# Kernel tuning notes

Hardware: AMD Instinct MI355X
Metric: run time of the kernel (lower is better)

## Reference

```python
import jax, jax.numpy as jnp
import numpy as np
import math

S, B, D_MODEL = 1024, 2, 1024
N_HEADS = 16
D_HEAD = D_MODEL // N_HEADS
C = 32  # compressed_len


def _xavier(key, shape):
    fan_in, fan_out = shape[-1], shape[-2] if len(shape) > 1 else shape[-1]
    limit = math.sqrt(6.0 / (fan_in + fan_out))
    return jax.random.uniform(key, shape, jnp.float32, -limit, limit)


def setup_inputs() -> dict:
    key = jax.random.key(0)
    ks = jax.random.split(key, 10)
    return {
        "x": jax.random.normal(ks[0], (S, B, D_MODEL), jnp.float32),
        "q_down": _xavier(ks[1], (C, D_MODEL)),
        "Wq": _xavier(ks[2], (D_MODEL, D_MODEL)),
        "bq": jnp.zeros((D_MODEL,), jnp.float32),
        "Wk": _xavier(ks[3], (D_MODEL, D_MODEL)),
        "bk": jnp.zeros((D_MODEL,), jnp.float32),
        "Wv": _xavier(ks[4], (D_MODEL, D_MODEL)),
        "bv": jnp.zeros((D_MODEL,), jnp.float32),
        "Wo": _xavier(ks[5], (D_MODEL, D_MODEL)),
        "bo": jnp.zeros((D_MODEL,), jnp.float32),
    }


def reference(x, q_down, Wq, bq, Wk, bk, Wv, bv, Wo, bo):
    # x: (s, b, d_model); causal=True, rope=None, dropout inactive (eval)
    s, b, d_model = x.shape
    h, dh = N_HEADS, D_HEAD
    scale = 1.0 / math.sqrt(dh)

    q_u = x @ Wq.T + bq                       # (s,b,dm)
    k_d = x @ Wk.T + bk
    v_d = x @ Wv.T + bv
    v_d_k = v_d @ Wk.T + bk
    v_d_v = v_d @ Wv.T + bv

    def heads(t):  # (s,b,dm) -> (b,h,s,dh)
        return t.reshape(s, b, h, dh).transpose(1, 2, 0, 3)

    q_u = heads(q_u) * scale
    k_d = heads(k_d)
    v_d_kv = jnp.concatenate([heads(v_d_k), heads(v_d_v)], axis=-1)  # (b,h,s,2dh)

    q_d = q_down.reshape(C, h, dh).transpose(1, 0, 2) * scale        # (h,c,dh)

    down = jnp.einsum('hcd,bhsd->bhcs', q_d, k_d)                    # (b,h,c,s)
    w = jnp.exp(down - jnp.max(down, axis=-1, keepdims=True))
    norm = jnp.cumsum(w, axis=-1)

    # (b,h,c,s,2dh): running compressed KV state
    kv_u = jnp.cumsum(w[..., None] * v_d_kv[:, :, None, :, :], axis=3) / norm[..., None]
    k_u, v_u = jnp.split(kv_u, 2, axis=-1)                           # each (b,h,c,s,dh)

    up = jnp.einsum('bhsd,bhcsd->bhsc', q_u, k_u)
    up = jax.nn.softmax(up, axis=-1)
    out = jnp.einsum('bhsc,bhcsd->bhsd', up, v_u)                    # (b,h,s,dh)

    out = out.transpose(2, 0, 1, 3).reshape(s, b, d_model)
    return out @ Wo.T + bo
```

## Files before the change

kernel.cpp:

```cpp
#include <hip/hip_runtime.h>
#include <cstdint>
#include <cstddef>

#define S_LEN 1024
#define BATCH 2
#define DM    1024
#define NH    16
#define DH    64
#define CC    32
#define SB    2048
#define TSD   128
#define NCHD  8

using short8 = __attribute__((ext_vector_type(8))) short;
using f32x4  = __attribute__((ext_vector_type(4))) float;

__device__ __forceinline__ float b2f(unsigned short u) {
    union { unsigned int i; float f; } v; v.i = ((unsigned int)u) << 16; return v.f;
}
__device__ __forceinline__ unsigned short f2b(float f) {
    union { float f; unsigned int i; } v; v.f = f;
    unsigned int x = v.i;
    unsigned int r = x + 0x7FFFu + ((x >> 16) & 1u);
    return (unsigned short)(r >> 16);
}
// ... 199 lines not shown
        __syncthreads();
    }

    const int f32o = (ga.mode == 0) ? 1 : (ga.mode == 1) ? 0 : (!isbf);
    const float sc = ga.scale;
#pragma unroll
    for (int j = 0; j < 2; ++j) {
        int col = n0 + wx * 32 + j * 16 + ln;
        float bv = ga.bias[col];
#pragma unroll
        for (int i = 0; i < 4; ++i) {
            int row0 = m0 + wy * 64 + i * 16 + lq * 4;
#pragma unroll
            for (int r = 0; r < 4; ++r) {
                float v = (acc[i][j][r] + bv) * sc;
                size_t idx = (size_t)(row0 + r) * N + col;
                if (f32o) ((float*)ga.out)[idx] = v;
                else      ((unsigned short*)ga.out)[idx] = f2b(v);
            }
        }
    }
}

__global__ __launch_bounds__(256) void k_down(const unsigned short* __restrict__ kd,
                                              const unsigned short* __restrict__ qd0,
                                              const unsigned short* __restrict__ qd1,
                                              const int* __restrict__ flag,
                                              float* __restrict__ wbuf,
                                              float* __restrict__ cmax,
                                              float* __restrict__ csum)
{
    const unsigned short* qdw = (*flag) ? qd1 : qd0;
    const int bh = blockIdx.x;
    const int b = bh >> 4, h = bh & 15;
    const int chunk = blockIdx.y;
    const int s0 = chunk * TSD;
    const int t = threadIdx.x;
    const int w = t >> 6, l = t & 63;
    const int ln = l & 15, lq = l >> 4;

    __shared__ __align__(16) unsigned short QD[32 * 72];
    __shared__ __align__(16) unsigned short KT[128 * 72];
    __shared__ float SS[32 * 132];
    __shared__ float pm[256];
    __shared__ float cmf[CC];

    {
        int r = t >> 3, cb = (t & 7) * 8;
        *(short8*)&QD[r * 72 + cb] = *(const short8*)&qdw[(size_t)r * DM + h * DH + cb];
    }
    for (int u = t; u < 128 * 8; u += 256) {
        int r = u >> 3, cb = (u & 7) * 8;
        *(short8*)&KT[r * 72 + cb] =
            *(const short8*)&kd[(size_t)((s0 + r) * BATCH + b) * DM + h * DH + cb];
    }
    __syncthreads();

    f32x4 accG[2][2] = {};
#pragma unroll
    for (int ks = 0; ks < 2; ++ks) {
        short8 a8[2], b8[2];
#pragma unroll
        for (int i = 0; i < 2; ++i)
            a8[i] = *(const short8*)&QD[(i * 16 + ln) * 72 + ks * 32 + lq * 8];
#pragma unroll
        for (int j = 0; j < 2; ++j)
            b8[j] = *(const short8*)&KT[(w * 32 + j * 16 + ln) * 72 + ks * 32 + lq * 8];
#pragma unroll
        for (int i = 0; i < 2; ++i)
#pragma unroll
            for (int j = 0; j < 2; ++j)
                accG[i][j] = __builtin_amdgcn_mfma_f32_16x16x32_bf16(a8[i], b8[j], accG[i][j], 0, 0, 0);
    }
#pragma unroll
    for (int i = 0; i < 2; ++i) {
#pragma unroll
        for (int j = 0; j < 2; ++j) {
            int sl = w * 32 + j * 16 + ln;
#pragma unroll
            for (int r = 0; r < 4; ++r) {
                int c = i * 16 + lq * 4 + r;
                float v = accG[i][j][r] * 0.125f;
                SS[c * 132 + sl] = v;
                wbuf[((size_t)bh * CC + c) * S_LEN + s0 + sl] = v;
            }
        }
    }
    __syncthreads();

    const int c = t >> 3, sub = t & 7;
    float lmax = -3.4e38f;
#pragma unroll
    for (int k = 0; k < 16; ++k) lmax = fmaxf(lmax, SS[c * 132 + sub * 16 + k]);
    lmax = fmaxf(lmax, __shfl_xor(lmax, 1));
    lmax = fmaxf(lmax, __shfl_xor(lmax, 2));
    lmax = fmaxf(lmax, __shfl_xor(lmax, 4));
    if (sub == 0) {
        cmf[c] = lmax;
        cmax[((size_t)bh * CC + c) * NCHD + chunk] = lmax;
    }
    __syncthreads();
    const float cm = cmf[c];
    float es = 0.f;
#pragma unroll
    for (int k = 0; k < 16; ++k) es += __expf(SS[c * 132 + sub * 16 + k] - cm);
    es += __shfl_xor(es, 1);
    es += __shfl_xor(es, 2);
    es += __shfl_xor(es, 4);
    if (sub == 0) csum[((size_t)bh * CC + c) * NCHD + chunk] = es;
}

__global__ __launch_bounds__(256) void k_wapply(const float* __restrict__ wbuf,
                                                const float* __restrict__ cmax,
                                                const float* __restrict__ csum,
                                                unsigned short* __restrict__ wb,
                                                unsigned short* __restrict__ wT,
                                                float* __restrict__ invn)
{
    const int bh = blockIdx.x, seg = blockIdx.y;
    const int t = threadIdx.x;
    __shared__ float gm[CC];
    __shared__ float basep[CC];
    __shared__ float psum[CC][9];
    __shared__ unsigned short wTt[128 * 40];
    __shared__ float invt[128 * 36];

    if (t < CC) {
        const size_t cb = (size_t)(bh * CC + t) * NCHD;
        float m = cmax[cb];
#pragma unroll
        for (int g = 1; g < NCHD; ++g) m = fmaxf(m, cmax[cb + g]);
        gm[t] = m;
        float bsum = 0.f;
        for (int k = 0; k < seg; ++k)
            bsum += csum[cb + k] * __expf(cmax[cb + k] - m);
        basep[t] = bsum;
    }
    __syncthreads();

    const int c = t >> 3, sub = t & 7;
    const float gmc = gm[c];
    const size_t rbase = (size_t)bh * 32768 + c * 1024 + seg * 128 + sub * 16;
    float w16[16];
    float s = 0.f;
#pragma unroll
    for (int i = 0; i < 16; ++i) {
        float v = __expf(wbuf[rbase + i] - gmc);
        w16[i] = v; s += v;
    }
    psum[c][sub] = s;
    short8 o0, o1;
#pragma unroll
    for (int i = 0; i < 8; ++i) { o0[i] = f2b(w16[i]); o1[i] = f2b(w16[8 + i]); }
    *(short8*)&wb[rbase] = o0;
    *(short8*)&wb[rbase + 8] = o1;
#pragma unroll
    for (int i = 0; i < 16; ++i) wTt[(sub * 16 + i) * 40 + c] = f2b(w16[i]);
    __syncthreads();

    float run = basep[c];
    for (int k = 0; k < sub; ++k) run += psum[c][k];
#pragma unroll
    for (int i = 0; i < 16; ++i) {
        run += w16[i];
        invt[(sub * 16 + i) * 36 + c] = 1.0f / fmaxf(run, 1e-30f);
    }
    __syncthreads();

    for (int u = t; u < 128 * 4; u += 256) {
        int r = u >> 2, cb = (u & 3) * 8;
        *(short8*)&wT[(size_t)bh * 32768 + (seg * 128 + r) * 32 + cb] =
            *(const short8*)&wTt[r * 40 + cb];
    }
    for (int u = t; u < 128 * 8; u += 256) {
        int r = u >> 3, cb = (u & 7) * 4;
        *(float4*)&invn[(size_t)bh * 32768 + (seg * 128 + r) * 32 + cb] =
            *(const float4*)&invt[r * 36 + cb];
    }
}

__global__ __launch_bounds__(256) void k_state(const unsigned short* __restrict__ wb,
                                               const unsigned short* __restrict__ vdk,
                                               const unsigned short* __restrict__ vdv,
                                               float* __restrict__ Mst,
                                               float* __restrict__ NTst)
{
    const int bh = blockIdx.x, ch = blockIdx.y;
    const int b = bh >> 4, h = bh & 15;
    const int s0 = ch * 64;
    const int t = threadIdx.x;
    const int w = t >> 6, l = t & 63;
    const int ln = l & 15, lq = l >> 4;
    __shared__ __align__(16) unsigned short Ws[32 * 72];
    __shared__ __align__(16) unsigned short T1[64 * 72];
    __shared__ __align__(16) unsigned short T2[64 * 72];
    __shared__ __align__(16) unsigned short KT[64 * 72];
    __shared__ __align__(16) unsigned short VT[64 * 72];

    for (int u = t; u < 32 * 8; u += 256) {
        int r = u >> 3, cb = (u & 7) * 8;
        *(short8*)&Ws[r * 72 + cb] = *(const short8*)&wb[(size_t)bh * 32768 + r * 1024 + s0 + cb];
    }
    for (int u = t; u < 64 * 8; u += 256) {
        int r = u >> 3, cb = (u & 7) * 8;
        *(short8*)&T1[r * 72 + cb] =
            *(const short8*)&vdk[(size_t)((s0 + r) * BATCH + b) * DM + h * DH + cb];
        *(short8*)&T2[r * 72 + cb] =
            *(const short8*)&vdv[(size_t)((s0 + r) * BATCH + b) * DM + h * DH + cb];
    }
    __syncthreads();
    for (int u = t; u < 64 * 8; u += 256) {
        int d = u >> 3, s8 = (u & 7) * 8;
        short8 o1, o2;
#pragma unroll
        for (int k = 0; k < 8; ++k) {
            o1[k] = T1[(s8 + k) * 72 + d];
            o2[k] = T2[(s8 + k) * 72 + d];
        }
        *(short8*)&KT[d * 72 + s8] = o1;
        *(short8*)&VT[d * 72 + s8] = o2;
    }
    __syncthreads();

    f32x4 accM[2] = {};
#pragma unroll
    for (int ks = 0; ks < 2; ++ks) {
        short8 b8 = *(const short8*)&KT[(w * 16 + ln) * 72 + ks * 32 + lq * 8];
#pragma unroll
        for (int i = 0; i < 2; ++i) {
            short8 a8 = *(const short8*)&Ws[(i * 16 + ln) * 72 + ks * 32 + lq * 8];
            accM[i] = __builtin_amdgcn_mfma_f32_16x16x32_bf16(a8, b8, accM[i], 0, 0, 0);
        }
    }
#pragma unroll
    for (int i = 0; i < 2; ++i)
#pragma unroll
        for (int r = 0; r < 4; ++r)
            Mst[((size_t)(bh * 16 + ch) * 32 + i * 16 + lq * 4 + r) * 64 + w * 16 + ln] = accM[i][r];

    f32x4 accN[2] = {};
#pragma unroll
    for (int ks = 0; ks < 2; ++ks) {
        short8 a8 = *(const short8*)&VT[(w * 16 + ln) * 72 + ks * 32 + lq * 8];
#pragma unroll
        for (int j = 0; j < 2; ++j) {
            short8 b8 = *(const short8*)&Ws[(j * 16 + ln) * 72 + ks * 32 + lq * 8];
            accN[j] = __builtin_amdgcn_mfma_f32_16x16x32_bf16(a8, b8, accN[j], 0, 0, 0);
        }
    }
#pragma unroll
    for (int j = 0; j < 2; ++j)
#pragma unroll
        for (int r = 0; r < 4; ++r)
            NTst[((size_t)(bh * 16 + ch) * 64 + w * 16 + lq * 4 + r) * 32 + j * 16 + ln] = accN[j][r];
}

__global__ __launch_bounds__(256) void k_prefix(const float* __restrict__ Mst,
                                                const float* __restrict__ NTst,
                                                unsigned short* __restrict__ Mcum,
                                                unsigned short* __restrict__ NTcum)
{
    const int bh = blockIdx.x;
    const float* src = blockIdx.y ? NTst : Mst;
    unsigned short* dst = blockIdx.y ? NTcum : Mcum;
    const int e0 = blockIdx.z * 512 + threadIdx.x * 2;
    float r0 = 0.f, r1 = 0.f;
#pragma unroll
    for (int ch = 0; ch < 16; ++ch) {
        size_t off = (size_t)(bh * 16 + ch) * 2048 + e0;
        ushort2 ob; ob.x = f2b(r0); ob.y = f2b(r1);
        *(ushort2*)&dst[off] = ob;
        float2 v = *(const float2*)&src[off];
        r0 += v.x; r1 += v.y;
    }
}

__global__ __launch_bounds__(256) void k_att(
    const unsigned short* __restrict__ qu,
    const unsigned short* __restrict__ vdk,
    const unsigned short* __restrict__ wb,
    const float* __restrict__ invn,
    const unsigned short* __restrict__ wT,
    const unsigned short* __restrict__ vdv,
    const unsigned short* __restrict__ Mcum,
    const unsigned short* __restrict__ NTcum,
    unsigned short* __restrict__ attout)
{
    const int bh = blockIdx.x, b = bh >> 4, h = bh & 15;
    const int qi = blockIdx.y;
    const int s0 = qi * 64;
    const int t = threadIdx.x;
    const int w = t >> 6, l = t & 63;
    const int wy = w >> 1, wx = w & 1;
    const int ln = l & 15, lq = l >> 4;

    __shared__ __align__(16) unsigned short Qs[64 * 72];
    __shared__ __align__(16) unsigned short Gs[64 * 72];
    __shared__ __align__(16) unsigned short Kd[64 * 72];
    __shared__ __align__(16) unsigned short Wd[32 * 72];
    __shared__ __align__(16) unsigned short WTd[64 * 40];
    __shared__ __align__(16) unsigned short VTd[64 * 72];
    __shared__ __align__(16) unsigned short Mc[32 * 72];
    __shared__ __align__(16) unsigned short Nc[64 * 40];

    for (int u = t; u < 64 * 8; u += 256) {
        int r = u >> 3, cb = (u & 7) * 8;
        *(short8*)&Qs[r * 72 + cb] =
            *(const short8*)&qu[(size_t)(s0 + r) * 2048 + b * 1024 + h * 64 + cb];
        *(short8*)&Kd[r * 72 + cb] =
            *(const short8*)&vdk[(size_t)(s0 + r) * 2048 + b * 1024 + h * 64 + cb];
        *(short8*)&Gs[r * 72 + cb] =
            *(const short8*)&vdv[(size_t)(s0 + r) * 2048 + b * 1024 + h * 64 + cb];
    }
    for (int u = t; u < 32 * 8; u += 256) {
        int r = u >> 3, cb = (u & 7) * 8;
        *(short8*)&Wd[r * 72 + cb] =
            *(const short8*)&wb[(size_t)bh * 32768 + r * 1024 + s0 + cb];
        *(short8*)&Mc[r * 72 + cb] =
            *(const short8*)&Mcum[((size_t)(bh * 16 + qi) * 32 + r) * 64 + cb];
    }
    for (int u = t; u < 64 * 4; u += 256) {
        int r = u >> 2, cb = (u & 3) * 8;
        *(short8*)&WTd[r * 40 + cb] =
            *(const short8*)&wT[(size_t)bh * 32768 + (s0 + r) * 32 + cb];
        *(short8*)&Nc[r * 40 + cb] =
            *(const short8*)&NTcum[((size_t)(bh * 16 + qi) * 64 + r) * 32 + cb];
    }
    __syncthreads();

    for (int u = t; u < 64 * 8; u += 256) {
        int d = u >> 3, s8 = (u & 7) * 8;
        short8 o;
#pragma unroll
        for (int k = 0; k < 8; ++k) o[k] = Gs[(s8 + k) * 72 + d];
        *(short8*)&VTd[d * 72 + s8] = o;
    }
    __syncthreads();

    {
        f32x4 accG[2][2] = {};
#pragma unroll
        for (int ks = 0; ks < 2; ++ks) {
            short8 a8[2], b8[2];
#pragma unroll
            for (int i = 0; i < 2; ++i)
                a8[i] = *(const short8*)&Qs[(wy * 32 + i * 16 + ln) * 72 + ks * 32 + lq * 8];
#pragma unroll
            for (int j = 0; j < 2; ++j)
                b8[j] = *(const short8*)&Kd[(wx * 32 + j * 16 + ln) * 72 + ks * 32 + lq * 8];
#pragma unroll
            for (int i = 0; i < 2; ++i)
#pragma unroll
                for (int j = 0; j < 2; ++j)
                    accG[i][j] = __builtin_amdgcn_mfma_f32_16x16x32_bf16(a8[i], b8[j], accG[i][j], 0, 0, 0);
        }
        __syncthreads();
#pragma unroll
        for (int i = 0; i < 2; ++i) {
            int row = wy * 32 + i * 16 + lq * 4;
#pragma unroll
            for (int j = 0; j < 2; ++j) {
                int col = wx * 32 + j * 16 + ln;
#pragma unroll
                for (int r = 0; r < 4; ++r) {
                    float v = accG[i][j][r];
                    if (col > row + r) v = 0.f;
                    Gs[(row + r) * 72 + col] = f2b(v);
                }
            }
        }
    }
    __syncthreads();

    f32x4 accU[2] = {};
#pragma unroll
    for (int ks = 0; ks < 2; ++ks) {
        short8 ga = *(const short8*)&Gs[(w * 16 + ln) * 72 + ks * 32 + lq * 8];
        short8 qa = *(const short8*)&Qs[(w * 16 + ln) * 72 + ks * 32 + lq * 8];
#pragma unroll
        for (int j = 0; j < 2; ++j) {
            short8 wf = *(const short8*)&Wd[(j * 16 + ln) * 72 + ks * 32 + lq * 8];
            short8 mf = *(const short8*)&Mc[(j * 16 + ln) * 72 + ks * 32 + lq * 8];
            accU[j] = __builtin_amdgcn_mfma_f32_16x16x32_bf16(ga, wf, accU[j], 0, 0, 0);
            accU[j] = __builtin_amdgcn_mfma_f32_16x16x32_bf16(qa, mf, accU[j], 0, 0, 0);
        }
    }
    __syncthreads();

    {
        int rowl = w * 16 + lq * 4;
#pragma unroll
        for (int r = 0; r < 4; ++r) {
            int srow = s0 + rowl + r;
            float inv0 = invn[(size_t)bh * 32768 + srow * 32 + ln];
            float inv1 = invn[(size_t)bh * 32768 + srow * 32 + 16 + ln];
            float l0 = accU[0][r] * inv0;
            float l1 = accU[1][r] * inv1;
            float m = fmaxf(l0, l1);
#pragma unroll
            for (int msk = 1; msk < 16; msk <<= 1) m = fmaxf(m, __shfl_xor(m, msk));
            float e0 = __expf(l0 - m), e1 = __expf(l1 - m);
            float Z = e0 + e1;
#pragma unroll
            for (int msk = 1; msk < 16; msk <<= 1) Z += __shfl_xor(Z, msk);
            float iz = 1.0f / Z;
            Qs[(rowl + r) * 40 + ln]      = f2b(e0 * iz * inv0);
            Qs[(rowl + r) * 40 + 16 + ln] = f2b(e1 * iz * inv1);
        }
    }
    __syncthreads();

    short8 pa[2];
#pragma unroll
    for (int i = 0; i < 2; ++i)
        pa[i] = *(const short8*)&Qs[(wy * 32 + i * 16 + ln) * 40 + lq * 8];
    {
        f32x4 accS[2][2] = {};
        short8 b8[2];
#pragma unroll
        for (int j = 0; j < 2; ++j)
            b8[j] = *(const short8*)&WTd[(wx * 32 + j * 16 + ln) * 40 + lq * 8];
#pragma unroll
        for (int i = 0; i < 2; ++i)
#pragma unroll
            for (int j = 0; j < 2; ++j)
                accS[i][j] = __builtin_amdgcn_mfma_f32_16x16x32_bf16(pa[i], b8[j], accS[i][j], 0, 0, 0);
#pragma unroll
        for (int i = 0; i < 2; ++i) {
            int row = wy * 32 + i * 16 + lq * 4;
#pragma unroll
            for (int j = 0; j < 2; ++j) {
                int col = wx * 32 + j * 16 + ln;
#pragma unroll
                for (int r = 0; r < 4; ++r) {
                    float v = accS[i][j][r];
                    if (col > row + r) v = 0.f;
                    Gs[(row + r) * 72 + col] = f2b(v);
                }
            }
        }
    }
    __syncthreads();

    {
        f32x4 accO[2][2] = {};
        short8 n8[2];
#pragma unroll
        for (int j = 0; j < 2; ++j)
            n8[j] = *(const short8*)&Nc[(wx * 32 + j * 16 + ln) * 40 + lq * 8];
#pragma unroll
        for (int i = 0; i < 2; ++i)
#pragma unroll
            for (int j = 0; j < 2; ++j)
                accO[i][j] = __builtin_amdgcn_mfma_f32_16x16x32_bf16(pa[i], n8[j], accO[i][j], 0, 0, 0);
#pragma unroll
        for (int ks = 0; ks < 2; ++ks) {
            short8 a8[2], b8[2];
#pragma unroll
            for (int i = 0; i < 2; ++i)
                a8[i] = *(const short8*)&Gs[(wy * 32 + i * 16 + ln) * 72 + ks * 32 + lq * 8];
#pragma unroll
            for (int j = 0; j < 2; ++j)
                b8[j] = *(const short8*)&VTd[(wx * 32 + j * 16 + ln) * 72 + ks * 32 + lq * 8];
#pragma unroll
            for (int i = 0; i < 2; ++i)
#pragma unroll
                for (int j = 0; j < 2; ++j)
                    accO[i][j] = __builtin_amdgcn_mfma_f32_16x16x32_bf16(a8[i], b8[j], accO[i][j], 0, 0, 0);
        }
#pragma unroll
        for (int i = 0; i < 2; ++i) {
            int rowb = s0 + wy * 32 + i * 16 + lq * 4;
#pragma unroll
            for (int j = 0; j < 2; ++j) {
                int d = wx * 32 + j * 16 + ln;
#pragma unroll
                for (int r = 0; r < 4; ++r)
                    attout[(size_t)(rowb + r) * 2048 + b * 1024 + h * 64 + d] = f2b(accO[i][j][r]);
            }
        }
    }
}

extern "C" void kernel_launch(void* const* d_in, const int* in_sizes, int n_in,
                              void* d_out, int out_size, void* d_ws, size_t ws_size,
                              hipStream_t stream)
{
    (void)in_sizes; (void)n_in; (void)out_size; (void)ws_size;
    char* ws = (char*)d_ws;
    const size_t MB = (size_t)1 << 20;
    const size_t KB = (size_t)1 << 10;
    unsigned short* attout = (unsigned short*)(ws + 0 * MB);
    unsigned short* q_u    = (unsigned short*)(ws + 4 * MB);
    unsigned short* k_d    = (unsigned short*)(ws + 8 * MB);
    unsigned short* v_dk   = (unsigned short*)(ws + 12 * MB);
    unsigned short* v_dv   = (unsigned short*)(ws + 16 * MB);
    float* wbuf = (float*)(ws + 20 * MB);
    unsigned short* wb  = (unsigned short*)(ws + 24 * MB);
    unsigned short* wT  = (unsigned short*)(ws + 26 * MB);
    float* invn = (float*)(ws + 28 * MB);
    float* Mst  = (float*)(ws + 32 * MB);
    float* NTst = (float*)(ws + 36 * MB);
    unsigned short* Mcum  = (unsigned short*)(ws + 40 * MB);
    unsigned short* NTcum = (unsigned short*)(ws + 42 * MB);
    unsigned short* xb  = (unsigned short*)(ws + 44 * MB);
    unsigned short* Wqb = (unsigned short*)(ws + 48 * MB);
    unsigned short* Wkb = (unsigned short*)(ws + 50 * MB);
    unsigned short* Wvb = (unsigned short*)(ws + 52 * MB);
    unsigned short* Wob = (unsigned short*)(ws + 54 * MB);
    unsigned short* v_d = (unsigned short*)(ws + 56 * MB);
    unsigned short* qdb = (unsigned short*)(ws + 62 * MB);
    float* biasf  = (float*)(ws + 62 * MB + 64 * KB);
    float* cmax   = (float*)(ws + 62 * MB + 192 * KB);
    float* csum   = (float*)(ws + 62 * MB + 256 * KB);
    int*   flag   = (int*)  (ws + 62 * MB + 320 * KB);

    const unsigned short* xraw  = (const unsigned short*)d_in[0];
    const unsigned short* qdraw = (const unsigned short*)d_in[1];
    const unsigned short* wqraw = (const unsigned short*)d_in[2];
    const unsigned short* wkraw = (const unsigned short*)d_in[4];
    const unsigned short* wvraw = (const unsigned short*)d_in[6];
    const unsigned short* woraw = (const unsigned short*)d_in[8];

    k_convert<<<1024, 256, 0, stream>>>(
        d_in[0], d_in[1], d_in[2], d_in[4], d_in[6], d_in[8],
        d_in[3], d_in[5], d_in[7], d_in[9],
        flag, xb, qdb, Wqb, Wkb, Wvb, Wob, biasf);

    const float* bqf = biasf;
    const float* bkf = biasf + 1024;
    const float* bvf = biasf + 2048;
    const float* bof = biasf + 3072;

    GArg gq { xb, xraw, Wqb, wqraw, bqf, (void*)q_u, 0.125f, 1 };
    GArg gk { xb, xraw, Wkb, wkraw, bkf, (void*)k_d, 1.0f, 1 };
    GArg gv { xb, xraw, Wvb, wvraw, bvf, (void*)v_d, 1.0f, 1 };
    gemm_bt<<<dim3(8, 16, 3), 256, 0, stream>>>(gq, gk, gv, gq, flag, SB, DM, DM);

    GArg gvk{ v_d, v_d, Wkb, wkraw, bkf, (void*)v_dk, 1.0f, 1 };
    GArg gvv{ v_d, v_d, Wvb, wvraw, bvf, (void*)v_dv, 1.0f, 1 };
    gemm_bt<<<dim3(8, 16, 2), 256, 0, stream>>>(gvk, gvv, gvk, gvk, flag, SB, DM, DM);

    k_down<<<dim3(32, NCHD), 256, 0, stream>>>(k_d, qdb, qdraw, flag, wbuf, cmax, csum);
    k_wapply<<<dim3(32, 8), 256, 0, stream>>>(wbuf, cmax, csum, wb, wT, invn);
    k_state<<<dim3(32, 16), 256, 0, stream>>>(wb, v_dk, v_dv, Mst, NTst);
    k_prefix<<<dim3(32, 2, 4), 256, 0, stream>>>(Mst, NTst, Mcum, NTcum);
    k_att<<<dim3(32, 16), 256, 0, stream>>>(q_u, v_dk, wb, invn, wT, v_dv, Mcum, NTcum, attout);

    GArg go{ attout, attout, Wob, woraw, bof, d_out, 1.0f, 2 };
    gemm_bt_n64<<<dim3(16, 16, 1), 256, 0, stream>>>(go, go, flag, SB, DM, DM);
}
```

Measured before the change: 189.4 us.

## Fuse mid-stage attention kernels into one cooperative persistent kernel with grid syncs

Replaces the five separate launches (down-projection scores, weight apply, per-chunk state, prefix sum, attention output) with a single cooperative kernel of 256 blocks that separates phases with grid-wide barriers. The fp32 score buffer wbuf is no longer written by the first phase, so one intermediate global round trip goes away. The aim is to remove launch gaps and tail effects between small kernels. In exchange the phases are forced onto a fixed 256-block grid with one block per CU, and every grid barrier costs a synchronisation.

```diff
diff --git a/kernel.cpp b/kernel.cpp
--- a/kernel.cpp
+++ b/kernel.cpp
@@ -1,6 +1,9 @@
 #include <hip/hip_runtime.h>
+#include <hip/hip_cooperative_groups.h>
 #include <cstdint>
 #include <cstddef>
+
+namespace cg = cooperative_groups;
 
 #define S_LEN 1024
 #define BATCH 2
@@ -246,462 +249,467 @@
     }
 }
 
-__global__ __launch_bounds__(256) void k_down(const unsigned short* __restrict__ kd,
-                                              const unsigned short* __restrict__ qd0,
-                                              const unsigned short* __restrict__ qd1,
-                                              const int* __restrict__ flag,
-                                              float* __restrict__ wbuf,
-                                              float* __restrict__ cmax,
-                                              float* __restrict__ csum)
+struct MidArgs {
+    const unsigned short* kd;
+    const unsigned short* qd0;
+    const unsigned short* qd1;
+    const int* flag;
+    float* cmax;
+    float* csum;
+    unsigned short* wb;
+    unsigned short* wT;
+    float* invn;
+    const unsigned short* vdk;
+    const unsigned short* vdv;
+    float* Mst;
+    float* NTst;
+    unsigned short* Mcum;
+    unsigned short* NTcum;
+    const unsigned short* qu;
+    unsigned short* attout;
+};
+
+__global__ __launch_bounds__(256, 1) void k_mid(MidArgs a)
 {
-    const unsigned short* qdw = (*flag) ? qd1 : qd0;
-    const int bh = blockIdx.x;
-    const int b = bh >> 4, h = bh & 15;
-    const int chunk = blockIdx.y;
-    const int s0 = chunk * TSD;
+    cg::grid_group grid = cg::this_grid();
+    __shared__ __align__(16) unsigned char SMEM[56320];
+
     const int t = threadIdx.x;
     const int w = t >> 6, l = t & 63;
     const int ln = l & 15, lq = l >> 4;
-
-    __shared__ __align__(16) unsigned short QD[32 * 72];
-    __shared__ __align__(16) unsigned short KT[128 * 72];
-    __shared__ float SS[32 * 132];
-    __shared__ float pm[256];
-    __shared__ float cmf[CC];
+    const int bh = blockIdx.x >> 3;
+    const int b = bh >> 4, h = bh & 15;
+    const int sub8 = blockIdx.x & 7;
+
+    float* SS = (float*)(SMEM);
 
     {
-        int r = t >> 3, cb = (t & 7) * 8;
-        *(short8*)&QD[r * 72 + cb] = *(const short8*)&qdw[(size_t)r * DM + h * DH + cb];
-    }
-    for (int u = t; u < 128 * 8; u += 256) {
-        int r = u >> 3, cb = (u & 7) * 8;
-        *(short8*)&KT[r * 72 + cb] =
-            *(const short8*)&kd[(size_t)((s0 + r) * BATCH + b) * DM + h * DH + cb];
-    }
-    __syncthreads();
-
-    f32x4 accG[2][2] = {};
-#pragma unroll
-    for (int ks = 0; ks < 2; ++ks) {
-        short8 a8[2], b8[2];
-#pragma unroll
-        for (int i = 0; i < 2; ++i)
-            a8[i] = *(const short8*)&QD[(i * 16 + ln) * 72 + ks * 32 + lq * 8];
-#pragma unroll
-        for (int j = 0; j < 2; ++j)
-            b8[j] = *(const short8*)&KT[(w * 32 + j * 16 + ln) * 72 + ks * 32 + lq * 8];
-#pragma unroll
-        for (int i = 0; i < 2; ++i)
-#pragma unroll
-            for (int j = 0; j < 2; ++j)
-                accG[i][j] = __builtin_amdgcn_mfma_f32_16x16x32_bf16(a8[i], b8[j], accG[i][j], 0, 0, 0);
-    }
-#pragma unroll
-    for (int i = 0; i < 2; ++i) {
-#pragma unroll
-        for (int j = 0; j < 2; ++j) {
-            int sl = w * 32 + j * 16 + ln;
-#pragma unroll
-            for (int r = 0; r < 4; ++r) {
-                int c = i * 16 + lq * 4 + r;
-                float v = accG[i][j][r] * 0.125f;
-                SS[c * 132 + sl] = v;
-                wbuf[((size_t)bh * CC + c) * S_LEN + s0 + sl] = v;
-            }
-        }
-    }
-    __syncthreads();
-
-    const int c = t >> 3, sub = t & 7;
-    float lmax = -3.4e38f;
-#pragma unroll
-    for (int k = 0; k < 16; ++k) lmax = fmaxf(lmax, SS[c * 132 + sub * 16 + k]);
-    lmax = fmaxf(lmax, __shfl_xor(lmax, 1));
-    lmax = fmaxf(lmax, __shfl_xor(lmax, 2));
-    lmax = fmaxf(lmax, __shfl_xor(lmax, 4));
-    if (sub == 0) {
-        cmf[c] = lmax;
-        cmax[((size_t)bh * CC + c) * NCHD + chunk] = lmax;
-    }
-    __syncthreads();
-    const float cm = cmf[c];
-    float es = 0.f;
-#pragma unroll
-    for (int k = 0; k < 16; ++k) es += __expf(SS[c * 132 + sub * 16 + k] - cm);
-    es += __shfl_xor(es, 1);
-    es += __shfl_xor(es, 2);
-    es += __shfl_xor(es, 4);
-    if (sub == 0) csum[((size_t)bh * CC + c) * NCHD + chunk] = es;
-}
-
-__global__ __launch_bounds__(256) void k_wapply(const float* __restrict__ wbuf,
-                                                const float* __restrict__ cmax,
-                                                const float* __restrict__ csum,
-                                                unsigned short* __restrict__ wb,
-                                                unsigned short* __restrict__ wT,
-                                                float* __restrict__ invn)
-{
-    const int bh = blockIdx.x, seg = blockIdx.y;
-    const int t = threadIdx.x;
-    __shared__ float gm[CC];
-    __shared__ float basep[CC];
-    __shared__ float psum[CC][9];
-    __shared__ unsigned short wTt[128 * 40];
-    __shared__ float invt[128 * 36];
-
-    if (t < CC) {
-        const size_t cb = (size_t)(bh * CC + t) * NCHD;
-        float m = cmax[cb];
-#pragma unroll
-        for (int g = 1; g < NCHD; ++g) m = fmaxf(m, cmax[cb + g]);
-        gm[t] = m;
-        float bsum = 0.f;
-        for (int k = 0; k < seg; ++k)
-            bsum += csum[cb + k] * __expf(cmax[cb + k] - m);
-        basep[t] = bsum;
-    }
-    __syncthreads();
-
-    const int c = t >> 3, sub = t & 7;
-    const float gmc = gm[c];
-    const size_t rbase = (size_t)bh * 32768 + c * 1024 + seg * 128 + sub * 16;
-    float w16[16];
-    float s = 0.f;
-#pragma unroll
-    for (int i = 0; i < 16; ++i) {
-        float v = __expf(wbuf[rbase + i] - gmc);
-        w16[i] = v; s += v;
-    }
-    psum[c][sub] = s;
-    short8 o0, o1;
-#pragma unroll
-    for (int i = 0; i < 8; ++i) { o0[i] = f2b(w16[i]); o1[i] = f2b(w16[8 + i]); }
-    *(short8*)&wb[rbase] = o0;
-    *(short8*)&wb[rbase + 8] = o1;
-#pragma unroll
-    for (int i = 0; i < 16; ++i) wTt[(sub * 16 + i) * 40 + c] = f2b(w16[i]);
-    __syncthreads();
-
-    float run = basep[c];
-    for (int k = 0; k < sub; ++k) run += psum[c][k];
-#pragma unroll
-    for (int i = 0; i < 16; ++i) {
-        run += w16[i];
-        invt[(sub * 16 + i) * 36 + c] = 1.0f / fmaxf(run, 1e-30f);
-    }
-    __syncthreads();
-
-    for (int u = t; u < 128 * 4; u += 256) {
-        int r = u >> 2, cb = (u & 3) * 8;
-        *(short8*)&wT[(size_t)bh * 32768 + (seg * 128 + r) * 32 + cb] =
-            *(const short8*)&wTt[r * 40 + cb];
-    }
-    for (int u = t; u < 128 * 8; u += 256) {
-        int r = u >> 3, cb = (u & 7) * 4;
-        *(float4*)&invn[(size_t)bh * 32768 + (seg * 128 + r) * 32 + cb] =
-            *(const float4*)&invt[r * 36 + cb];
-    }
-}
-
-__global__ __launch_bounds__(256) void k_state(const unsigned short* __restrict__ wb,
-                                               const unsigned short* __restrict__ vdk,
-                                               const unsigned short* __restrict__ vdv,
-                                               float* __restrict__ Mst,
-                                               float* __restrict__ NTst)
-{
-    const int bh = blockIdx.x, ch = blockIdx.y;
-    const int b = bh >> 4, h = bh & 15;
-    const int s0 = ch * 64;
-    const int t = threadIdx.x;
-    const int w = t >> 6, l = t & 63;
-    const int ln = l & 15, lq = l >> 4;
-    __shared__ __align__(16) unsigned short Ws[32 * 72];
-    __shared__ __align__(16) unsigned short T1[64 * 72];
-    __shared__ __align__(16) unsigned short T2[64 * 72];
-    __shared__ __align__(16) unsigned short KT[64 * 72];
-    __shared__ __align__(16) unsigned short VT[64 * 72];
-
-    for (int u = t; u < 32 * 8; u += 256) {
-        int r = u >> 3, cb = (u & 7) * 8;
-        *(short8*)&Ws[r * 72 + cb] = *(const short8*)&wb[(size_t)bh * 32768 + r * 1024 + s0 + cb];
-    }
-    for (int u = t; u < 64 * 8; u += 256) {
-        int r = u >> 3, cb = (u & 7) * 8;
-        *(short8*)&T1[r * 72 + cb] =
-            *(const short8*)&vdk[(size_t)((s0 + r) * BATCH + b) * DM + h * DH + cb];
-        *(short8*)&T2[r * 72 + cb] =
-            *(const short8*)&vdv[(size_t)((s0 + r) * BATCH + b) * DM + h * DH + cb];
-    }
-    __syncthreads();
-    for (int u = t; u < 64 * 8; u += 256) {
-        int d = u >> 3, s8 = (u & 7) * 8;
-        short8 o1, o2;
-#pragma unroll
-        for (int k = 0; k < 8; ++k) {
-            o1[k] = T1[(s8 + k) * 72 + d];
-            o2[k] = T2[(s8 + k) * 72 + d];
-        }
-        *(short8*)&KT[d * 72 + s8] = o1;
-        *(short8*)&VT[d * 72 + s8] = o2;
-    }
-    __syncthreads();
-
-    f32x4 accM[2] = {};
-#pragma unroll
-    for (int ks = 0; ks < 2; ++ks) {
-        short8 b8 = *(const short8*)&KT[(w * 16 + ln) * 72 + ks * 32 + lq * 8];
-#pragma unroll
-        for (int i = 0; i < 2; ++i) {
-            short8 a8 = *(const short8*)&Ws[(i * 16 + ln) * 72 + ks * 32 + lq * 8];
-            accM[i] = __builtin_amdgcn_mfma_f32_16x16x32_bf16(a8, b8, accM[i], 0, 0, 0);
-        }
-    }
-#pragma unroll
-    for (int i = 0; i < 2; ++i)
-#pragma unroll
-        for (int r = 0; r < 4; ++r)
-            Mst[((size_t)(bh * 16 + ch) * 32 + i * 16 + lq * 4 + r) * 64 + w * 16 + ln] = accM[i][r];
-
-    f32x4 accN[2] = {};
-#pragma unroll
-    for (int ks = 0; ks < 2; ++ks) {
-        short8 a8 = *(const short8*)&VT[(w * 16 + ln) * 72 + ks * 32 + lq * 8];
-#pragma unroll
-        for (int j = 0; j < 2; ++j) {
-            short8 b8 = *(const short8*)&Ws[(j * 16 + ln) * 72 + ks * 32 + lq * 8];
-            accN[j] = __builtin_amdgcn_mfma_f32_16x16x32_bf16(a8, b8, accN[j], 0, 0, 0);
-        }
-    }
-#pragma unroll
-    for (int j = 0; j < 2; ++j)
-#pragma unroll
-        for (int r = 0; r < 4; ++r)
-            NTst[((size_t)(bh * 16 + ch) * 64 + w * 16 + lq * 4 + r) * 32 + j * 16 + ln] = accN[j][r];
-}
-
-__global__ __launch_bounds__(256) void k_prefix(const float* __restrict__ Mst,
-                                                const float* __restrict__ NTst,
-                                                unsigned short* __restrict__ Mcum,
-                                                unsigned short* __restrict__ NTcum)
-{
-    const int bh = blockIdx.x;
-    const float* src = blockIdx.y ? NTst : Mst;
-    unsigned short* dst = blockIdx.y ? NTcum : Mcum;
-    const int e0 = blockIdx.z * 512 + threadIdx.x * 2;
-    float r0 = 0.f, r1 = 0.f;
-#pragma unroll
-    for (int ch = 0; ch < 16; ++ch) {
-        size_t off = (size_t)(bh * 16 + ch) * 2048 + e0;
-        ushort2 ob; ob.x = f2b(r0); ob.y = f2b(r1);
-        *(ushort2*)&dst[off] = ob;
-        float2 v = *(const float2*)&src[off];
-        r0 += v.x; r1 += v.y;
-    }
-}
-
-__global__ __launch_bounds__(256) void k_att(
-    const unsigned short* __restrict__ qu,
-    const unsigned short* __restrict__ vdk,
-    const unsigned short* __restrict__ wb,
-    const float* __restrict__ invn,
-    const unsigned short* __restrict__ wT,
-    const unsigned short* __restrict__ vdv,
-    const unsigned short* __restrict__ Mcum,
-    const unsigned short* __restrict__ NTcum,
-    unsigned short* __restrict__ attout)
-{
-    const int bh = blockIdx.x, b = bh >> 4, h = bh & 15;
-    const int qi = blockIdx.y;
-    const int s0 = qi * 64;
-    const int t = threadIdx.x;
-    const int w = t >> 6, l = t & 63;
-    const int wy = w >> 1, wx = w & 1;
-    const int ln = l & 15, lq = l >> 4;
-
-    __shared__ __align__(16) unsigned short Qs[64 * 72];
-    __shared__ __align__(16) unsigned short Gs[64 * 72];
-    __shared__ __align__(16) unsigned short Kd[64 * 72];
-    __shared__ __align__(16) unsigned short Wd[32 * 72];
-    __shared__ __align__(16) unsigned short WTd[64 * 40];
-    __shared__ __align__(16) unsigned short VTd[64 * 72];
-    __shared__ __align__(16) unsigned short Mc[32 * 72];
-    __shared__ __align__(16) unsigned short Nc[64 * 40];
-
-    for (int u = t; u < 64 * 8; u += 256) {
-        int r = u >> 3, cb = (u & 7) * 8;
-        *(short8*)&Qs[r * 72 + cb] =
-            *(const short8*)&qu[(size_t)(s0 + r) * 2048 + b * 1024 + h * 64 + cb];
-        *(short8*)&Kd[r * 72 + cb] =
-            *(const short8*)&vdk[(size_t)(s0 + r) * 2048 + b * 1024 + h * 64 + cb];
-        *(short8*)&Gs[r * 72 + cb] =
-            *(const short8*)&vdv[(size_t)(s0 + r) * 2048 + b * 1024 + h * 64 + cb];
-    }
-    for (int u = t; u < 32 * 8; u += 256) {
-        int r = u >> 3, cb = (u & 7) * 8;
-        *(short8*)&Wd[r * 72 + cb] =
-            *(const short8*)&wb[(size_t)bh * 32768 + r * 1024 + s0 + cb];
-        *(short8*)&Mc[r * 72 + cb] =
-            *(const short8*)&Mcum[((size_t)(bh * 16 + qi) * 32 + r) * 64 + cb];
-    }
-    for (int u = t; u < 64 * 4; u += 256) {
-        int r = u >> 2, cb = (u & 3) * 8;
-        *(short8*)&WTd[r * 40 + cb] =
-            *(const short8*)&wT[(size_t)bh * 32768 + (s0 + r) * 32 + cb];
-        *(short8*)&Nc[r * 40 + cb] =
-            *(const short8*)&NTcum[((size_t)(bh * 16 + qi) * 64 + r) * 32 + cb];
-    }
-    __syncthreads();
-
-    for (int u = t; u < 64 * 8; u += 256) {
-        int d = u >> 3, s8 = (u & 7) * 8;
-        short8 o;
-#pragma unroll
-        for (int k = 0; k < 8; ++k) o[k] = Gs[(s8 + k) * 72 + d];
-        *(short8*)&VTd[d * 72 + s8] = o;
-    }
-    __syncthreads();
-
-    {
+        unsigned short* QD  = (unsigned short*)(SMEM + 16896);
+        unsigned short* KT  = (unsigned short*)(SMEM + 21504);
+        float* cmf          = (float*)(SMEM + 39936);
+
+        const unsigned short* qdw = (*a.flag) ? a.qd1 : a.qd0;
+        const int chunk = sub8;
+        const int s0 = chunk * TSD;
+
+        {
+            int r = t >> 3, cb = (t & 7) * 8;
+            *(short8*)&QD[r * 72 + cb] = *(const short8*)&qdw[(size_t)r * DM + h * DH + cb];
+        }
+        for (int u = t; u < 128 * 8; u += 256) {
+            int r = u >> 3, cb = (u & 7) * 8;
+            *(short8*)&KT[r * 72 + cb] =
+                *(const short8*)&a.kd[(size_t)((s0 + r) * BATCH + b) * DM + h * DH + cb];
+        }
+        __syncthreads();
+
         f32x4 accG[2][2] = {};
 #pragma unroll
         for (int ks = 0; ks < 2; ++ks) {
             short8 a8[2], b8[2];
 #pragma unroll
             for (int i = 0; i < 2; ++i)
-                a8[i] = *(const short8*)&Qs[(wy * 32 + i * 16 + ln) * 72 + ks * 32 + lq * 8];
+                a8[i] = *(const short8*)&QD[(i * 16 + ln) * 72 + ks * 32 + lq * 8];
 #pragma unroll
             for (int j = 0; j < 2; ++j)
-                b8[j] = *(const short8*)&Kd[(wx * 32 + j * 16 + ln) * 72 + ks * 32 + lq * 8];
+                b8[j] = *(const short8*)&KT[(w * 32 + j * 16 + ln) * 72 + ks * 32 + lq * 8];
 #pragma unroll
             for (int i = 0; i < 2; ++i)
 #pragma unroll
                 for (int j = 0; j < 2; ++j)
                     accG[i][j] = __builtin_amdgcn_mfma_f32_16x16x32_bf16(a8[i], b8[j], accG[i][j], 0, 0, 0);
         }
-        __syncthreads();
 #pragma unroll
         for (int i = 0; i < 2; ++i) {
-            int row = wy * 32 + i * 16 + lq * 4;
 #pragma unroll
             for (int j = 0; j < 2; ++j) {
-                int col = wx * 32 + j * 16 + ln;
+                int sl = w * 32 + j * 16 + ln;
 #pragma unroll
                 for (int r = 0; r < 4; ++r) {
-                    float v = accG[i][j][r];
-                    if (col > row + r) v = 0.f;
-                    Gs[(row + r) * 72 + col] = f2b(v);
-                }
-            }
-        }
-    }
-    __syncthreads();
-
-    f32x4 accU[2] = {};
-#pragma unroll
-    for (int ks = 0; ks < 2; ++ks) {
-        short8 ga = *(const short8*)&Gs[(w * 16 + ln) * 72 + ks * 32 + lq * 8];
-        short8 qa = *(const short8*)&Qs[(w * 16 + ln) * 72 + ks * 32 + lq * 8];
-#pragma unroll
-        for (int j = 0; j < 2; ++j) {
-            short8 wf = *(const short8*)&Wd[(j * 16 + ln) * 72 + ks * 32 + lq * 8];
-            short8 mf = *(const short8*)&Mc[(j * 16 + ln) * 72 + ks * 32 + lq * 8];
-            accU[j] = __builtin_amdgcn_mfma_f32_16x16x32_bf16(ga, wf, accU[j], 0, 0, 0);
-            accU[j] = __builtin_amdgcn_mfma_f32_16x16x32_bf16(qa, mf, accU[j], 0, 0, 0);
-        }
-    }
-    __syncthreads();
+                    int c = i * 16 + lq * 4 + r;
+                    SS[c * 132 + sl] = accG[i][j][r] * 0.125f;
+                }
+            }
+        }
+        __syncthreads();
+
+        const int c = t >> 3, sb = t & 7;
+        float lmax = -3.4e38f;
+#pragma unroll
+        for (int k = 0; k < 16; ++k) lmax = fmaxf(lmax, SS[c * 132 + sb * 16 + k]);
+        lmax = fmaxf(lmax, __shfl_xor(lmax, 1));
+        lmax = fmaxf(lmax, __shfl_xor(lmax, 2));
+        lmax = fmaxf(lmax, __shfl_xor(lmax, 4));
+        if (sb == 0) {
+            cmf[c] = lmax;
+            a.cmax[((size_t)bh * CC + c) * NCHD + chunk] = lmax;
+        }
+        __syncthreads();
+        const float cm = cmf[c];
+        float es = 0.f;
+#pragma unroll
+        for (int k = 0; k < 16; ++k) es += __expf(SS[c * 132 + sb * 16 + k] - cm);
+        es += __shfl_xor(es, 1);
+        es += __shfl_xor(es, 2);
+        es += __shfl_xor(es, 4);
+        if (sb == 0) a.csum[((size_t)bh * CC + c) * NCHD + chunk] = es;
+    }
+    __threadfence();
+    grid.sync();
 
     {
-        int rowl = w * 16 + lq * 4;
-#pragma unroll
-        for (int r = 0; r < 4; ++r) {
-            int srow = s0 + rowl + r;
-            float inv0 = invn[(size_t)bh * 32768 + srow * 32 + ln];
-            float inv1 = invn[(size_t)bh * 32768 + srow * 32 + 16 + ln];
-            float l0 = accU[0][r] * inv0;
-            float l1 = accU[1][r] * inv1;
-            float m = fmaxf(l0, l1);
-#pragma unroll
-            for (int msk = 1; msk < 16; msk <<= 1) m = fmaxf(m, __shfl_xor(m, msk));
-            float e0 = __expf(l0 - m), e1 = __expf(l1 - m);
-            float Z = e0 + e1;
-#pragma unroll
-            for (int msk = 1; msk < 16; msk <<= 1) Z += __shfl_xor(Z, msk);
-            float iz = 1.0f / Z;
-            Qs[(rowl + r) * 40 + ln]      = f2b(e0 * iz * inv0);
-            Qs[(rowl + r) * 40 + 16 + ln] = f2b(e1 * iz * inv1);
-        }
-    }
-    __syncthreads();
-
-    short8 pa[2];
-#pragma unroll
-    for (int i = 0; i < 2; ++i)
-        pa[i] = *(const short8*)&Qs[(wy * 32 + i * 16 + ln) * 40 + lq * 8];
+        float* gm            = (float*)(SMEM + 16896);
+        float* basep         = (float*)(SMEM + 17024);
+        float* psum          = (float*)(SMEM + 17152);
+        unsigned short* wTt  = (unsigned short*)(SMEM + 18304);
+        float* invt          = (float*)(SMEM + 28544);
+
+        const int seg = sub8;
+
+        if (t < CC) {
+            const size_t cb = (size_t)(bh * CC + t) * NCHD;
+            float m = a.cmax[cb];
+#pragma unroll
+            for (int g = 1; g < NCHD; ++g) m = fmaxf(m, a.cmax[cb + g]);
+            gm[t] = m;
+            float bsum = 0.f;
+            for (int k = 0; k < seg; ++k)
+                bsum += a.csum[cb + k] * __expf(a.cmax[cb + k] - m);
+            basep[t] = bsum;
+        }
+        __syncthreads();
+
+        const int c = t >> 3, sb = t & 7;
+        const float gmc = gm[c];
+        const size_t rbase = (size_t)bh * 32768 + c * 1024 + seg * 128 + sb * 16;
+        float w16[16];
+        float s = 0.f;
+#pragma unroll
+        for (int i = 0; i < 16; ++i) {
+            float v = __expf(SS[c * 132 + sb * 16 + i] - gmc);
+            w16[i] = v; s += v;
+        }
+        psum[c * 9 + sb] = s;
+        short8 o0, o1;
+#pragma unroll
+        for (int i = 0; i < 8; ++i) { o0[i] = f2b(w16[i]); o1[i] = f2b(w16[8 + i]); }
+        *(short8*)&a.wb[rbase] = o0;
+        *(short8*)&a.wb[rbase + 8] = o1;
+#pragma unroll
+        for (int i = 0; i < 16; ++i) wTt[(sb * 16 + i) * 40 + c] = f2b(w16[i]);
+        __syncthreads();
+
+        float run = basep[c];
+        for (int k = 0; k < sb; ++k) run += psum[c * 9 + k];
+#pragma unroll
+        for (int i = 0; i < 16; ++i) {
+            run += w16[i];
+            invt[(sb * 16 + i) * 36 + c] = 1.0f / fmaxf(run, 1e-30f);
+        }
+        __syncthreads();
+
+        for (int u = t; u < 128 * 4; u += 256) {
+            int r = u >> 2, cb2 = (u & 3) * 8;
+            *(short8*)&a.wT[(size_t)bh * 32768 + (seg * 128 + r) * 32 + cb2] =
+                *(const short8*)&wTt[r * 40 + cb2];
+        }
+        for (int u = t; u < 128 * 8; u += 256) {
+            int r = u >> 3, cb2 = (u & 7) * 4;
+            *(float4*)&a.invn[(size_t)bh * 32768 + (seg * 128 + r) * 32 + cb2] =
+                *(const float4*)&invt[r * 36 + cb2];
+        }
+    }
+    __threadfence();
+    grid.sync();
+
     {
-        f32x4 accS[2][2] = {};
-        short8 b8[2];
-#pragma unroll
-        for (int j = 0; j < 2; ++j)
-            b8[j] = *(const short8*)&WTd[(wx * 32 + j * 16 + ln) * 40 + lq * 8];
-#pragma unroll
-        for (int i = 0; i < 2; ++i)
+        unsigned short* Ws  = (unsigned short*)(SMEM + 0);
+        unsigned short* T1  = (unsigned short*)(SMEM + 4608);
+        unsigned short* T2  = (unsigned short*)(SMEM + 13824);
+        unsigned short* KT2 = (unsigned short*)(SMEM + 23040);
+        unsigned short* VT  = (unsigned short*)(SMEM + 32256);
+
+        for (int rep = 0; rep < 2; ++rep) {
+            const int ch = sub8 * 2 + rep;
+            const int s0 = ch * 64;
+
+            for (int u = t; u < 32 * 8; u += 256) {
+                int r = u >> 3, cb = (u & 7) * 8;
+                *(short8*)&Ws[r * 72 + cb] =
+                    *(const short8*)&a.wb[(size_t)bh * 32768 + r * 1024 + s0 + cb];
+            }
+            for (int u = t; u < 64 * 8; u += 256) {
+                int r = u >> 3, cb = (u & 7) * 8;
+                *(short8*)&T1[r * 72 + cb] =
+                    *(const short8*)&a.vdk[(size_t)((s0 + r) * BATCH + b) * DM + h * DH + cb];
+                *(short8*)&T2[r * 72 + cb] =
+                    *(const short8*)&a.vdv[(size_t)((s0 + r) * BATCH + b) * DM + h * DH + cb];
+            }
+            __syncthreads();
+            for (int u = t; u < 64 * 8; u += 256) {
+                int d = u >> 3, s8 = (u & 7) * 8;
+                short8 o1, o2;
+#pragma unroll
+                for (int k = 0; k < 8; ++k) {
+                    o1[k] = T1[(s8 + k) * 72 + d];
+                    o2[k] = T2[(s8 + k) * 72 + d];
+                }
+                *(short8*)&KT2[d * 72 + s8] = o1;
+                *(short8*)&VT[d * 72 + s8] = o2;
+            }
+            __syncthreads();
+
+            f32x4 accM[2] = {};
+#pragma unroll
+            for (int ks = 0; ks < 2; ++ks) {
+                short8 b8 = *(const short8*)&KT2[(w * 16 + ln) * 72 + ks * 32 + lq * 8];
+#pragma unroll
+                for (int i = 0; i < 2; ++i) {
+                    short8 a8 = *(const short8*)&Ws[(i * 16 + ln) * 72 + ks * 32 + lq * 8];
+                    accM[i] = __builtin_amdgcn_mfma_f32_16x16x32_bf16(a8, b8, accM[i], 0, 0, 0);
+                }
+            }
+#pragma unroll
+            for (int i = 0; i < 2; ++i)
+#pragma unroll
+                for (int r = 0; r < 4; ++r)
+                    a.Mst[((size_t)(bh * 16 + ch) * 32 + i * 16 + lq * 4 + r) * 64 + w * 16 + ln] = accM[i][r];
+
+            f32x4 accN[2] = {};
+#pragma unroll
+            for (int ks = 0; ks < 2; ++ks) {
+                short8 a8 = *(const short8*)&VT[(w * 16 + ln) * 72 + ks * 32 + lq * 8];
+#pragma unroll
+                for (int j = 0; j < 2; ++j) {
+                    short8 b8 = *(const short8*)&Ws[(j * 16 + ln) * 72 + ks * 32 + lq * 8];
+                    accN[j] = __builtin_amdgcn_mfma_f32_16x16x32_bf16(a8, b8, accN[j], 0, 0, 0);
+                }
+            }
 #pragma unroll
             for (int j = 0; j < 2; ++j)
-                accS[i][j] = __builtin_amdgcn_mfma_f32_16x16x32_bf16(pa[i], b8[j], accS[i][j], 0, 0, 0);
-#pragma unroll
-        for (int i = 0; i < 2; ++i) {
-            int row = wy * 32 + i * 16 + lq * 4;
-#pragma unroll
-            for (int j = 0; j < 2; ++j) {
-                int col = wx * 32 + j * 16 + ln;
+#pragma unroll
+                for (int r = 0; r < 4; ++r)
+                    a.NTst[((size_t)(bh * 16 + ch) * 64 + w * 16 + lq * 4 + r) * 32 + j * 16 + ln] = accN[j][r];
+            __syncthreads();
+        }
+    }
+    __threadfence();
+    grid.sync();
+
+    {
+        const int y  = (blockIdx.x >> 2) & 1;
+        const int zz = blockIdx.x & 3;
+        const int bhp = blockIdx.x >> 3;
+        const float* src = y ? a.NTst : a.Mst;
+        unsigned short* dst = y ? a.NTcum : a.Mcum;
+        const int e0 = zz * 512 + t * 2;
+        float r0 = 0.f, r1 = 0.f;
+#pragma unroll
+        for (int ch = 0; ch < 16; ++ch) {
+            size_t off = (size_t)(bhp * 16 + ch) * 2048 + e0;
+            ushort2 ob; ob.x = f2b(r0); ob.y = f2b(r1);
+            *(ushort2*)&dst[off] = ob;
+            float2 v = *(const float2*)&src[off];
+            r0 += v.x; r1 += v.y;
+        }
+    }
+    __threadfence();
+    grid.sync();
+
+    {
+        unsigned short* Qs  = (unsigned short*)(SMEM + 0);
+        unsigned short* Gs  = (unsigned short*)(SMEM + 9216);
+        unsigned short* Kd  = (unsigned short*)(SMEM + 18432);
+        unsigned short* Wd  = (unsigned short*)(SMEM + 27648);
+        unsigned short* WTd = (unsigned short*)(SMEM + 32256);
+        unsigned short* VTd = (unsigned short*)(SMEM + 37376);
+        unsigned short* Mc  = (unsigned short*)(SMEM + 46592);
+        unsigned short* Nc  = (unsigned short*)(SMEM + 51200);
+
+        const int wy = w >> 1, wx = w & 1;
+
+        for (int rep = 0; rep < 2; ++rep) {
+            const int qi = sub8 * 2 + rep;
+            const int s0 = qi * 64;
+
+            for (int u = t; u < 64 * 8; u += 256) {
+                int r = u >> 3, cb = (u & 7) * 8;
+                *(short8*)&Qs[r * 72 + cb] =
+                    *(const short8*)&a.qu[(size_t)(s0 + r) * 2048 + b * 1024 + h * 64 + cb];
+                *(short8*)&Kd[r * 72 + cb] =
+                    *(const short8*)&a.vdk[(size_t)(s0 + r) * 2048 + b * 1024 + h * 64 + cb];
+                *(short8*)&Gs[r * 72 + cb] =
+                    *(const short8*)&a.vdv[(size_t)(s0 + r) * 2048 + b * 1024 + h * 64 + cb];
+            }
+            for (int u = t; u < 32 * 8; u += 256) {
+                int r = u >> 3, cb = (u & 7) * 8;
+                *(short8*)&Wd[r * 72 + cb] =
+                    *(const short8*)&a.wb[(size_t)bh * 32768 + r * 1024 + s0 + cb];
+                *(short8*)&Mc[r * 72 + cb] =
+                    *(const short8*)&a.Mcum[((size_t)(bh * 16 + qi) * 32 + r) * 64 + cb];
+            }
+            for (int u = t; u < 64 * 4; u += 256) {
+                int r = u >> 2, cb = (u & 3) * 8;
+                *(short8*)&WTd[r * 40 + cb] =
+                    *(const short8*)&a.wT[(size_t)bh * 32768 + (s0 + r) * 32 + cb];
+                *(short8*)&Nc[r * 40 + cb] =
+                    *(const short8*)&a.NTcum[((size_t)(bh * 16 + qi) * 64 + r) * 32 + cb];
+            }
+            __syncthreads();
+
+            for (int u = t; u < 64 * 8; u += 256) {
+                int d = u >> 3, s8 = (u & 7) * 8;
+                short8 o;
+#pragma unroll
+                for (int k = 0; k < 8; ++k) o[k] = Gs[(s8 + k) * 72 + d];
+                *(short8*)&VTd[d * 72 + s8] = o;
+            }
+            __syncthreads();
+
+            {
+                f32x4 accG[2][2] = {};
+#pragma unroll
+                for (int ks = 0; ks < 2; ++ks) {
+                    short8 a8[2], b8[2];
+#pragma unroll
+                    for (int i = 0; i < 2; ++i)
+                        a8[i] = *(const short8*)&Qs[(wy * 32 + i * 16 + ln) * 72 + ks * 32 + lq * 8];
+#pragma unroll
+                    for (int j = 0; j < 2; ++j)
+                        b8[j] = *(const short8*)&Kd[(wx * 32 + j * 16 + ln) * 72 + ks * 32 + lq * 8];
+#pragma unroll
+                    for (int i = 0; i < 2; ++i)
+#pragma unroll
+                        for (int j = 0; j < 2; ++j)
+                            accG[i][j] = __builtin_amdgcn_mfma_f32_16x16x32_bf16(a8[i], b8[j], accG[i][j], 0, 0, 0);
+                }
+                __syncthreads();
+#pragma unroll
+                for (int i = 0; i < 2; ++i) {
+                    int row = wy * 32 + i * 16 + lq * 4;
+#pragma unroll
+                    for (int j = 0; j < 2; ++j) {
+                        int col = wx * 32 + j * 16 + ln;
+#pragma unroll
+                        for (int r = 0; r < 4; ++r) {
+                            float v = accG[i][j][r];
+                            if (col > row + r) v = 0.f;
+                            Gs[(row + r) * 72 + col] = f2b(v);
+                        }
+                    }
+                }
+            }
+            __syncthreads();
+
+            f32x4 accU[2] = {};
+#pragma unroll
+            for (int ks = 0; ks < 2; ++ks) {
+                short8 ga = *(const short8*)&Gs[(w * 16 + ln) * 72 + ks * 32 + lq * 8];
+                short8 qa = *(const short8*)&Qs[(w * 16 + ln) * 72 + ks * 32 + lq * 8];
+#pragma unroll
+                for (int j = 0; j < 2; ++j) {
+                    short8 wf = *(const short8*)&Wd[(j * 16 + ln) * 72 + ks * 32 + lq * 8];
+                    short8 mf = *(const short8*)&Mc[(j * 16 + ln) * 72 + ks * 32 + lq * 8];
+                    accU[j] = __builtin_amdgcn_mfma_f32_16x16x32_bf16(ga, wf, accU[j], 0, 0, 0);
+                    accU[j] = __builtin_amdgcn_mfma_f32_16x16x32_bf16(qa, mf, accU[j], 0, 0, 0);
+                }
+            }
+            __syncthreads();
+
+            {
+                int rowl = w * 16 + lq * 4;
 #pragma unroll
                 for (int r = 0; r < 4; ++r) {
-                    float v = accS[i][j][r];
-                    if (col > row + r) v = 0.f;
-                    Gs[(row + r) * 72 + col] = f2b(v);
-                }
-            }
-        }
-    }
-    __syncthreads();
-
-    {
-        f32x4 accO[2][2] = {};
-        short8 n8[2];
-#pragma unroll
-        for (int j = 0; j < 2; ++j)
-            n8[j] = *(const short8*)&Nc[(wx * 32 + j * 16 + ln) * 40 + lq * 8];
-#pragma unroll
-        for (int i = 0; i < 2; ++i)
-#pragma unroll
-            for (int j = 0; j < 2; ++j)
-                accO[i][j] = __builtin_amdgcn_mfma_f32_16x16x32_bf16(pa[i], n8[j], accO[i][j], 0, 0, 0);
-#pragma unroll
-        for (int ks = 0; ks < 2; ++ks) {
-            short8 a8[2], b8[2];
+                    int srow = s0 + rowl + r;
+                    float inv0 = a.invn[(size_t)bh * 32768 + srow * 32 + ln];
+                    float inv1 = a.invn[(size_t)bh * 32768 + srow * 32 + 16 + ln];
+                    float l0 = accU[0][r] * inv0;
+                    float l1 = accU[1][r] * inv1;
+                    float m = fmaxf(l0, l1);
+#pragma unroll
+                    for (int msk = 1; msk < 16; msk <<= 1) m = fmaxf(m, __shfl_xor(m, msk));
+                    float e0 = __expf(l0 - m), e1 = __expf(l1 - m);
+                    float Z = e0 + e1;
+#pragma unroll
+                    for (int msk = 1; msk < 16; msk <<= 1) Z += __shfl_xor(Z, msk);
+                    float iz = 1.0f / Z;
+                    Qs[(rowl + r) * 40 + ln]      = f2b(e0 * iz * inv0);
+                    Qs[(rowl + r) * 40 + 16 + ln] = f2b(e1 * iz * inv1);
+                }
+            }
+            __syncthreads();
+
+            short8 pa[2];
 #pragma unroll
             for (int i = 0; i < 2; ++i)
-                a8[i] = *(const short8*)&Gs[(wy * 32 + i * 16 + ln) * 72 + ks * 32 + lq * 8];
-#pragma unroll
-            for (int j = 0; j < 2; ++j)
-                b8[j] = *(const short8*)&VTd[(wx * 32 + j * 16 + ln) * 72 + ks * 32 + lq * 8];
-#pragma unroll
-            for (int i = 0; i < 2; ++i)
+                pa[i] = *(const short8*)&Qs[(wy * 32 + i * 16 + ln) * 40 + lq * 8];
+            {
+                f32x4 accS[2][2] = {};
+                short8 b8[2];
 #pragma unroll
                 for (int j = 0; j < 2; ++j)
-                    accO[i][j] = __builtin_amdgcn_mfma_f32_16x16x32_bf16(a8[i], b8[j], accO[i][j], 0, 0, 0);
-        }
-#pragma unroll
-        for (int i = 0; i < 2; ++i) {
-            int rowb = s0 + wy * 32 + i * 16 + lq * 4;
-#pragma unroll
-            for (int j = 0; j < 2; ++j) {
-                int d = wx * 32 + j * 16 + ln;
-#pragma unroll
-                for (int r = 0; r < 4; ++r)
-                    attout[(size_t)(rowb + r) * 2048 + b * 1024 + h * 64 + d] = f2b(accO[i][j][r]);
-            }
+                    b8[j] = *(const short8*)&WTd[(wx * 32 + j * 16 + ln) * 40 + lq * 8];
+#pragma unroll
+                for (int i = 0; i < 2; ++i)
+#pragma unroll
+                    for (int j = 0; j < 2; ++j)
+                        accS[i][j] = __builtin_amdgcn_mfma_f32_16x16x32_bf16(pa[i], b8[j], accS[i][j], 0, 0, 0);
+#pragma unroll
+                for (int i = 0; i < 2; ++i) {
+                    int row = wy * 32 + i * 16 + lq * 4;
+#pragma unroll
+                    for (int j = 0; j < 2; ++j) {
+                        int col = wx * 32 + j * 16 + ln;
+#pragma unroll
+                        for (int r = 0; r < 4; ++r) {
+                            float v = accS[i][j][r];
+                            if (col > row + r) v = 0.f;
+                            Gs[(row + r) * 72 + col] = f2b(v);
+                        }
+                    }
+                }
+            }
+            __syncthreads();
+
+            {
+                f32x4 accO[2][2] = {};
+                short8 n8[2];
+#pragma unroll
+                for (int j = 0; j < 2; ++j)
+                    n8[j] = *(const short8*)&Nc[(wx * 32 + j * 16 + ln) * 40 + lq * 8];
+#pragma unroll
+                for (int i = 0; i < 2; ++i)
+#pragma unroll
+                    for (int j = 0; j < 2; ++j)
+                        accO[i][j] = __builtin_amdgcn_mfma_f32_16x16x32_bf16(pa[i], n8[j], accO[i][j], 0, 0, 0);
+#pragma unroll
+                for (int ks = 0; ks < 2; ++ks) {
+                    short8 a8[2], b8[2];
+#pragma unroll
+                    for (int i = 0; i < 2; ++i)
+                        a8[i] = *(const short8*)&Gs[(wy * 32 + i * 16 + ln) * 72 + ks * 32 + lq * 8];
+#pragma unroll
+                    for (int j = 0; j < 2; ++j)
+                        b8[j] = *(const short8*)&VTd[(wx * 32 + j * 16 + ln) * 72 + ks * 32 + lq * 8];
+#pragma unroll
+                    for (int i = 0; i < 2; ++i)
+#pragma unroll
+                        for (int j = 0; j < 2; ++j)
+                            accO[i][j] = __builtin_amdgcn_mfma_f32_16x16x32_bf16(a8[i], b8[j], accO[i][j], 0, 0, 0);
+                }
+#pragma unroll
+                for (int i = 0; i < 2; ++i) {
+                    int rowb = s0 + wy * 32 + i * 16 + lq * 4;
+#pragma unroll
+                    for (int j = 0; j < 2; ++j) {
+                        int d = wx * 32 + j * 16 + ln;
+#pragma unroll
+                        for (int r = 0; r < 4; ++r)
+                            a.attout[(size_t)(rowb + r) * 2048 + b * 1024 + h * 64 + d] = f2b(accO[i][j][r]);
+                    }
+                }
+            }
+            __syncthreads();
         }
     }
 }
@@ -719,7 +727,6 @@
     unsigned short* k_d    = (unsigned short*)(ws + 8 * MB);
     unsigned short* v_dk   = (unsigned short*)(ws + 12 * MB);
     unsigned short* v_dv   = (unsigned short*)(ws + 16 * MB);
-    float* wbuf = (float*)(ws + 20 * MB);
     unsigned short* wb  = (unsigned short*)(ws + 24 * MB);
     unsigned short* wT  = (unsigned short*)(ws + 26 * MB);
     float* invn = (float*)(ws + 28 * MB);
@@ -765,11 +772,10 @@
     GArg gvv{ v_d, v_d, Wvb, wvraw, bvf, (void*)v_dv, 1.0f, 1 };
     gemm_bt<<<dim3(8, 16, 2), 256, 0, stream>>>(gvk, gvv, gvk, gvk, flag, SB, DM, DM);
 
-    k_down<<<dim3(32, NCHD), 256, 0, stream>>>(k_d, qdb, qdraw, flag, wbuf, cmax, csum);
-    k_wapply<<<dim3(32, 8), 256, 0, stream>>>(wbuf, cmax, csum, wb, wT, invn);
-    k_state<<<dim3(32, 16), 256, 0, stream>>>(wb, v_dk, v_dv, Mst, NTst);
-    k_prefix<<<dim3(32, 2, 4), 256, 0, stream>>>(Mst, NTst, Mcum, NTcum);
-    k_att<<<dim3(32, 16), 256, 0, stream>>>(q_u, v_dk, wb, invn, wT, v_dv, Mcum, NTcum, attout);
+    MidArgs ma{ k_d, qdb, qdraw, flag, cmax, csum, wb, wT, invn,
+                v_dk, v_dv, Mst, NTst, Mcum, NTcum, q_u, attout };
+    void* kargs[] = { (void*)&ma };
+    hipLaunchCooperativeKernel((const void*)k_mid, dim3(256), dim3(256), kargs, 0, stream);
 
     GArg go{ attout, attout, Wob, woraw, bof, d_out, 1.0f, 2 };
     gemm_bt_n64<<<dim3(16, 16, 1), 256, 0, stream>>>(go, go, flag, SB, DM, DM);
```

Result: slower. 424.9 us (+124.3%).
